# Performance work log

Measured on AMD Instinct MI355X. Metric: run time of the kernel, lower is better.

Reference implementation:

```python
import jax, jax.numpy as jnp
from jax import lax
import numpy as np

SCALES = [1.0, 0.9, 0.8, 0.7, 0.6]
SOFTMAX_SCALE = 10.0
RES_SCALE = 1.0
EPS = 1e-4  # escape_NaN buffer


def prelu(x, a):
    # torch nn.PReLU with a single shared parameter a
    return jnp.where(x >= 0, x, a * x)


def conv1x1(x, W, b):
    # x: [B,Cin,H,W], W: [Cout,Cin], b: [Cout]
    return jnp.einsum('oi,bihw->bohw', W, x) + b[None, :, None, None]


def extract_patches(x):
    # x: [B,C,H,W] -> [B, H*W, C, 3, 3]; 'same' padding (pad 1), stride 1,
    # matching F.unfold channel ordering (C, kh, kw) and row-major spatial order.
    B, C, H, W = x.shape
    p = jnp.pad(x, ((0, 0), (0, 0), (1, 1), (1, 1)))
    shifts = [p[:, :, i:i + H, j:j + W] for i in range(3) for j in range(3)]
    pat = jnp.stack(shifts, axis=-1)                      # [B,C,H,W,9]
    pat = pat.reshape(B, C, H, W, 3, 3)
    return pat.transpose(0, 2, 3, 1, 4, 5).reshape(B, H * W, C, 3, 3)


def setup_inputs() -> dict:
    key = jax.random.key(0)
    ks = jax.random.split(key, 7)
    B, C, H, W = 4, 64, 48, 48
    red = 2
    x = jax.random.normal(ks[0], (B, C, H, W), jnp.float32)
    # conv_match_L_base: 1x1 conv 64->32 + PReLU
    Wb = jax.random.normal(ks[1], (C // red, C), jnp.float32) * 0.05
    bb = jax.random.normal(ks[2], (C // red,), jnp.float32) * 0.05
    ab = jnp.asarray(0.25, jnp.float32)
    # conv_match: 1x1 conv 64->32 + PReLU
    Wm = jax.random.normal(ks[3], (C // red, C), jnp.float32) * 0.05
    bm = jax.random.normal(ks[4], (C // red,), jnp.float32) * 0.05
    am = jnp.asarray(0.25, jnp.float32)
    # conv_assembly: 1x1 conv 64->64 + PReLU
    Wa = jax.random.normal(ks[5], (C, C), jnp.float32) * 0.05
    ba = jax.random.normal(ks[6], (C,), jnp.float32) * 0.05
    aa = jnp.asarray(0.25, jnp.float32)
    return {"x": x, "Wb": Wb, "bb": bb, "ab": ab,
            "Wm": Wm, "bm": bm, "am": am,
            "Wa": Wa, "ba": ba, "aa": aa}


def reference(x, Wb, bb, ab, Wm, bm, am, Wa, ba, aa):
    B, C, H, W = x.shape
    match_base = prelu(conv1x1(x, Wb, bb), ab)  # [B,32,H,W]

    w_list, raw_list = [], []
    for s in SCALES:
        if s != 1.0:
            Hs, Ws = int(H * s), int(W * s)
            ref = jax.image.resize(x, (B, C, Hs, Ws), 'bilinear', antialias=False)
        else:
            ref = x
        base = prelu(conv1x1(ref, Wa, ba), aa)   # [B,64,Hs,Ws]
        mat = prelu(conv1x1(ref, Wm, bm), am)    # [B,32,Hs,Ws]
        raw_list.append(extract_patches(base))   # [B,Ls,64,3,3]
        w_list.append(extract_patches(mat))      # [B,Ls,32,3,3]

    wall = jnp.concatenate(w_list, axis=1)       # [B,N,32,3,3]
    rawall = jnp.concatenate(raw_list, axis=1)   # [B,N,64,3,3]
    norm = jnp.maximum(jnp.sqrt(jnp.sum(wall * wall, axis=(2, 3, 4), keepdims=True)), EPS)
    wn = wall / norm

    dn = ('NCHW', 'OIHW', 'NCHW')

    def per_sample(xb, wb, rb):
        # xb: [32,H,W], wb: [N,32,3,3], rb: [N,64,3,3]
        scores = lax.conv_general_dilated(xb[None], wb, (1, 1), ((1, 1), (1, 1)),
                                          dimension_numbers=dn)       # [1,N,H,W]
        attn = jax.nn.softmax(scores * SOFTMAX_SCALE, axis=1)
        # conv_transpose2d(attn, rb, stride=1, padding=1) == conv with flipped,
        # channel-swapped kernel and padding 1
        kt = jnp.flip(rb, axis=(2, 3)).transpose(1, 0, 2, 3)           # [64,N,3,3]
        out = lax.conv_general_dilated(attn, kt, (1, 1), ((1, 1), (1, 1)),
                                       dimension_numbers=dn)           # [1,64,H,W]
        return out[0] / 4.0

    y = jax.vmap(per_sample)(match_base, wn, rawall)  # [B,64,H,W]
    return y + x * RES_SCALE
```

## Files before the change

### kernel.cpp

```cpp
#include <hip/hip_runtime.h>
#include <hip/hip_bf16.h>
#include <hip/hip_fp16.h>

typedef __half h16;
typedef _Float16 f16;
typedef f16 f16x8 __attribute__((ext_vector_type(8)));
typedef __attribute__((ext_vector_type(4))) float f32x4;

#define NB 4
#define NCH 64
#define HW 2304
#define NP 7470
#define NPAD 7552
#define NT 236
#define NT2 118
#define NBLK 59
#define SW2 NPAD

__device__ __forceinline__ float us2f(unsigned short u){
  unsigned v = (unsigned)u << 16; float f; __builtin_memcpy(&f, &v, 4); return f;
}
__device__ __forceinline__ void gl16(const void* g, void* l){
  __builtin_amdgcn_global_load_lds((const __attribute__((address_space(1))) unsigned int*)g,
                                   (__attribute__((address_space(3))) unsigned int*)l, 16, 0, 0);
}

__device__ __forceinline__ void n_decode(int n, int& off, int& d, int& y, int& x){
  if (n < 2304)      { off = 0;    d = 48; }
  else if (n < 4153) { off = 2304; d = 43; }
  else if (n < 5597) { off = 4153; d = 38; }
  else if (n < 6686) { off = 5597; d = 33; }
  else               { off = 6686; d = 28; }
  int l = n - off; y = l / d; x = l - y * d;
}

__global__ __launch_bounds__(256) void k_detect(const void* __restrict__ x, int* __restrict__ flag){
  const unsigned short* u = (const unsigned short*)x;
  int tid = threadIdx.x;
  int c = 0;
  for (int i = tid; i < 8192; i += 256){
    float v = us2f(u[i]);
    float a = fabsf(v);
    if (v == 0.f || (a > 1e-5f && a < 1e3f)) c++;
  }
  #pragma unroll
  for (int o = 1; o < 64; o <<= 1) c += __shfl_xor(c, o);
  __shared__ int wr[4];
  if ((tid & 63) == 0) wr[tid >> 6] = c;
  __syncthreads();
  if (tid == 0) flag[0] = ((wr[0]+wr[1]+wr[2]+wr[3]) > 7000) ? 1 : 0;
}

struct CanonArgs { const void* src[10]; float* dst[10]; int end[10]; };

__global__ __launch_bounds__(256) void k_canon_all(CanonArgs a, int tot, const int* __restrict__ flag){
  int id = blockIdx.x * 256 + threadIdx.x;
  if (id >= tot) return;
  int k = 0;
  while (id >= a.end[k]) k++;
  int local = id - (k ? a.end[k-1] : 0);
  float v;
  if (flag[0]) v = us2f(((const unsigned short*)a.src[k])[local]);
  else         v = ((const float*)a.src[k])[local];
  a.dst[k][local] = v;
}

__global__ __launch_bounds__(256) void k_resize(const float* __restrict__ x, h16* __restrict__ xs){
  int id = blockIdx.x * 256 + threadIdx.x;
  if (id >= NB * NCH * NP) return;
  int b = id / (NCH*NP), rem = id - b*(NCH*NP);
  int c = rem / NP, n = rem - c*NP;
  int off, d, y, xx; n_decode(n, off, d, y, xx);
  const float* pc = x + ((size_t)b * NCH + c) * HW;
  float v;
  if (off == 0){
    v = pc[y*48 + xx];
  } else {
    float cy = (y + 0.5f) * (48.0f / (float)d) - 0.5f;
    float cx = (xx + 0.5f) * (48.0f / (float)d) - 0.5f;
    int y0 = (int)floorf(cy), x0 = (int)floorf(cx);
    float fy = cy - (float)y0, fx = cx - (float)x0;
    int y1 = min(y0 + 1, 47), x1 = min(x0 + 1, 47);
    y0 = max(y0, 0); x0 = max(x0, 0);
    v = (1.f-fy)*((1.f-fx)*pc[y0*48+x0] + fx*pc[y0*48+x1])
      + fy*((1.f-fx)*pc[y1*48+x0] + fx*pc[y1*48+x1]);
  }
  xs[id] = __float2half(v);
}

template<bool OB>
__global__ __launch_bounds__(256) void k_conv1x1(const h16* __restrict__ in, const float* __restrict__ Wt,
    const float* __restrict__ bias, const float* __restrict__ alpha, void* __restrict__ outv,
    int npix, int cout, size_t in_bstride, size_t out_bstride, int rs_in, int rs_out){
  __shared__ float Wl[64*64];
  __shared__ float it[64][64];
  int b = blockIdx.y;
  int n0 = blockIdx.x * 64;
  int tid = threadIdx.x;
  const h16* ib = in + (size_t)b * in_bstride;
  for (int i = tid; i < cout * 64; i += 256) Wl[i] = Wt[i];
  for (int i = tid; i < 64 * 64; i += 256){
    int ci = i >> 6, nn = i & 63;
    int n = n0 + nn;
    it[ci][nn] = (n < npix) ? __half2float(ib[(size_t)ci * rs_in + n]) : 0.f;
  }
  __syncthreads();
  float al = alpha[0];
  for (int oi = tid; oi < cout * 64; oi += 256){
    int co = oi >> 6, nn = oi & 63;
    float acc = bias[co];
    #pragma unroll
    for (int ci = 0; ci < 64; ci++) acc = fmaf(Wl[co*64+ci], it[ci][nn], acc);
    acc = acc >= 0.f ? acc : al * acc;
    int n = n0 + nn;
    if (n < npix){
      size_t idx = (size_t)b * out_bstride + (size_t)co * rs_out + n;
      if constexpr (OB) ((h16*)outv)[idx] = __float2half(acc);
      else              ((float*)outv)[idx] = acc;
    }
  }
}

__global__ __launch_bounds__(256) void k_sq(const float* __restrict__ mat, float* __restrict__ q){
  int id = blockIdx.x * 256 + threadIdx.x;
  if (id >= NB * NP) return;
  int b = id / NP, n = id - b * NP;
  const float* mp = mat + (size_t)b * 32 * NP + n;
  float s = 0.f;
  #pragma unroll
  for (int c = 0; c < 32; c++){ float v = mp[(size_t)c * NP]; s += v * v; }
  q[id] = s;
}

__global__ __launch_bounds__(256) void k_ninv(const float* __restrict__ q, float* __restrict__ ninv){
  int id = blockIdx.x * 256 + threadIdx.x;
  if (id >= NB * NP) return;
  int b = id / NP, n = id - b * NP;
  int off, d, y, x; n_decode(n, off, d, y, x);
  const float* qb = q + (size_t)b * NP + off;
  float s = 0.f;
  #pragma unroll
  for (int dy = -1; dy <= 1; dy++){
    int yy = y + dy; if (yy < 0 || yy >= d) continue;
    #pragma unroll
    for (int dx = -1; dx <= 1; dx++){
      int xx = x + dx; if (xx < 0 || xx >= d) continue;
      s += qb[yy * d + xx];
    }
  }
  ninv[id] = 1.f / fmaxf(sqrtf(s), 1e-4f);
}

__global__ __launch_bounds__(256) void k_packU(const float* __restrict__ mb, h16* __restrict__ U){
  int id = blockIdx.x * 256 + threadIdx.x;
  if (id >= NB * HW * 288) return;
  int b = id / (HW*288), rem = id - b*(HW*288);
  int p = rem / 288, k = rem - p * 288;
  int c = k / 9, r = k - c * 9, kh = r / 3, kw = r - kh * 3;
  int y = p / 48 + kh - 1, x = (p % 48) + kw - 1;
  float v = 0.f;
  if (y >= 0 && y < 48 && x >= 0 && x < 48)
    v = mb[((size_t)b * 32 + c) * HW + y * 48 + x];
  U[id] = __float2half(v);
}

__global__ __launch_bounds__(256) void k_packW(const float* __restrict__ mat, const float* __restrict__ ninv,
                                               h16* __restrict__ Wp, int b0, int g){
  int id = blockIdx.x * 256 + threadIdx.x;
  if (id >= g * NPAD * 288) return;
  int bg = id / (NPAD*288), rem = id - bg*(NPAD*288);
  int n = rem / 288, k = rem - n * 288;
  float v = 0.f;
  if (n < NP){
    int b = b0 + bg;
    int c = k / 9, r = k - c * 9, kh = r / 3, kw = r - kh * 3;
    int off, d, y, x; n_decode(n, off, d, y, x);
    int yy = y + kh - 1, xx = x + kw - 1;
    if (yy >= 0 && yy < d && xx >= 0 && xx < d)
      v = mat[((size_t)b * 32 + c) * NP + off + yy * d + xx] * 10.f * ninv[(size_t)b*NP + n];
  }
  Wp[id] = __float2half(v);
}

__global__ __launch_bounds__(256) void k_packR(const h16* __restrict__ src, h16* __restrict__ dst){
  int id = blockIdx.x * 256 + threadIdx.x;
  if (id >= NB * NT * 576 * 32) return;
  int b = id / (NT*576*32), rem = id - b*(NT*576*32);
  int t = rem / (576*32), rem2 = rem - t*(576*32);
  int j = rem2 / 32, kl = rem2 - j*32;
  int n = t*32 + kl;
  h16 v = __float2half(0.f);
  if (n < NP){
    int c = j / 9, r = j - c * 9, kh = r / 3, kw = r - kh * 3;
    int off, d, y, x; n_decode(n, off, d, y, x);
    int yy = y + kh - 1, xx = x + kw - 1;
    if (yy >= 0 && yy < d && xx >= 0 && xx < d)
      v = src[((size_t)b * 64 + c) * NP + off + yy * d + xx];
  }
  dst[id] = v;
}

__global__ __launch_bounds__(512) void k_gemm1m(const f16* __restrict__ U, const f16* __restrict__ Wp,
    h16* __restrict__ S16, float* __restrict__ Pm, float* __restrict__ Ps, int b0){
  int nwg = gridDim.x;
  int p = blockIdx.x;
  int qc = nwg >> 3, rc = nwg & 7, xcd = p & 7;
  int L = (xcd < rc ? xcd*(qc+1) : rc*(qc+1) + (xcd - rc)*qc) + (p >> 3);
  int my = L % 18; int t1 = L / 18; int nb = t1 % NBLK; int bg = t1 / NBLK;
  int b = b0 + bg;
  int m0 = my * 128, n0 = nb * 128;
  int tid = threadIdx.x, l = tid & 63, w = tid >> 6;
  int wm = w >> 1, wn = w & 1;
  int ch = l >> 4, cl = l & 15;
  __shared__ __align__(16) char smem[51200];
  float* mredp = (float*)(smem + 49152);
  float* sredp = (float*)(smem + 50176);
  f32x4 acc[2][4] = {};
  const f16* Ub = U + ((size_t)b * HW + m0) * 288;
  const f16* Wb = Wp + ((size_t)bg * NPAD + n0) * 288;
  int abyte[2], bbyte[4];
  #pragma unroll
  for (int mt = 0; mt < 2; mt++){
    int lr = wm*32 + mt*16 + cl;
    abyte[mt] = lr*64 + ((ch ^ ((lr>>1)&3))<<4);
  }
  #pragma unroll
  for (int nt = 0; nt < 4; nt++){
    int lr = wn*64 + nt*16 + cl;
    bbyte[nt] = lr*64 + ((ch ^ ((lr>>1)&3))<<4);
  }
  int srow = tid >> 2, scs = (tid & 3) ^ ((srow >> 1) & 3);
  auto STAGE1 = [&](int t, int bi){
    gl16(Ub + (size_t)srow*288 + t*32 + scs*8, smem + bi*8192 + tid*16);
    gl16(Wb + (size_t)srow*288 + t*32 + scs*8, smem + 24576 + bi*8192 + tid*16);
  };
  STAGE1(0, 0);
  STAGE1(1, 1);
  __syncthreads();
  int cur = 0;
  for (int t = 0; t < 9; ++t){
    int nx = cur + 2; if (nx >= 3) nx -= 3;
    if (t + 2 < 9){
      STAGE1(t + 2, nx);
      asm volatile("s_waitcnt vmcnt(4)" ::: "memory");
    } else if (t + 1 < 9){
      asm volatile("s_waitcnt vmcnt(2)" ::: "memory");
    } else {
      asm volatile("s_waitcnt vmcnt(0)" ::: "memory");
    }
    __builtin_amdgcn_s_barrier();
    asm volatile("" ::: "memory");
    const char* Ac = smem + cur*8192;
    const char* Bc = smem + 24576 + cur*8192;
    __builtin_amdgcn_s_setprio(1);
    f16x8 a[2], bv[4];
    #pragma unroll
    for (int mt = 0; mt < 2; mt++) a[mt] = *reinterpret_cast<const f16x8*>(Ac + abyte[mt]);
    #pragma unroll
    for (int nt = 0; nt < 4; nt++) bv[nt] = *reinterpret_cast<const f16x8*>(Bc + bbyte[nt]);
    #pragma unroll
    for (int mt = 0; mt < 2; mt++)
      #pragma unroll
      for (int nt = 0; nt < 4; nt++)
        acc[mt][nt] = __builtin_amdgcn_mfma_f32_16x16x32_f16(a[mt], bv[nt], acc[mt][nt], 0, 0, 0);
    __builtin_amdgcn_s_setprio(0);
    asm volatile("s_waitcnt lgkmcnt(0)" ::: "memory");
    __builtin_amdgcn_s_barrier();
    cur = cur + 1; if (cur >= 3) cur -= 3;
  }
  #pragma unroll
  for (int mt = 0; mt < 2; mt++)
    #pragma unroll
    for (int i = 0; i < 4; i++){
      float v = -3e38f;
      #pragma unroll
      for (int nt = 0; nt < 4; nt++){
        int gn = n0 + wn*64 + nt*16 + cl;
        float t = acc[mt][nt][i];
        v = fmaxf(v, (gn < NP) ? t : -3e38f);
      }
      v = fmaxf(v, __shfl_xor(v, 1));
      v = fmaxf(v, __shfl_xor(v, 2));
      v = fmaxf(v, __shfl_xor(v, 4));
      v = fmaxf(v, __shfl_xor(v, 8));
      if (cl == 0) mredp[(wm*32 + mt*16 + ch*4 + i)*2 + wn] = v;
    }
  __syncthreads();
  {
    h16* Tl = (h16*)smem;
    #pragma unroll
    for (int mt = 0; mt < 2; mt++)
      #pragma unroll
      for (int i = 0; i < 4; i++){
        int r = wm*32 + mt*16 + ch*4 + i;
        float Ml = fmaxf(mredp[r*2+0], mredp[r*2+1]);
        float s = 0.f;
        #pragma unroll
        for (int nt = 0; nt < 4; nt++){
          int c = wn*64 + nt*16 + cl;
          int gn = n0 + c;
          float e = (gn < NP) ? __expf(acc[mt][nt][i] - Ml) : 0.f;
          Tl[r*132 + c] = __float2half(e);
          s += e;
        }
        s += __shfl_xor(s, 1);
        s += __shfl_xor(s, 2);
        s += __shfl_xor(s, 4);
        s += __shfl_xor(s, 8);
        if (cl == 0) sredp[r*2 + wn] = s;
      }
  }
  __syncthreads();
  if (tid < 128){
    float Mf = fmaxf(mredp[tid*2+0], mredp[tid*2+1]);
    float Lg = sredp[tid*2+0] + sredp[tid*2+1];
    size_t o = ((size_t)bg*HW + m0 + tid)*NBLK + nb;
    Pm[o] = Mf; Ps[o] = Lg;
  }
  {
    const h16* Tl = (const h16*)smem;
    #pragma unroll
    for (int rep = 0; rep < 4; rep++){
      int idx = tid + rep*512;
      int j0 = idx >> 4, qq = idx & 15;
      uint4 v = *reinterpret_cast<const uint4*>((const char*)Tl + j0*264 + qq*16);
      h16* dst = S16 + ((size_t)bg*HW + m0 + j0)*SW2 + n0 + qq*8;
      *reinterpret_cast<uint4*>(dst) = v;
    }
  }
}

__global__ __launch_bounds__(256) void k_sfac(const float* __restrict__ Pm, const float* __restrict__ Ps,
                                              float* __restrict__ Fac, int gc){
  int rid = blockIdx.x * 4 + (threadIdx.x >> 6);
  int lane = threadIdx.x & 63;
  if (rid >= gc * HW) return;
  const float* pm = Pm + (size_t)rid * NBLK;
  const float* ps = Ps + (size_t)rid * NBLK;
  float mv = (lane < NBLK) ? pm[lane] : -3e38f;
  float sv = (lane < NBLK) ? ps[lane] : 0.f;
  float M = mv;
  #pragma unroll
  for (int o = 1; o < 64; o <<= 1) M = fmaxf(M, __shfl_xor(M, o));
  float e = (lane < NBLK) ? __expf(mv - M) : 0.f;
  float c = e * sv;
  #pragma unroll
  for (int o = 1; o < 64; o <<= 1) c += __shfl_xor(c, o);
  float inv = 1.f / c;
  if (lane < NBLK) Fac[(size_t)rid * NBLK + lane] = e * inv;
}

__global__ __launch_bounds__(512) void k_gemm2n(const f16* __restrict__ S16, const f16* __restrict__ RpT,
    const float* __restrict__ Fac, h16* __restrict__ T, int b0){
  int nwg = gridDim.x;
  int p = blockIdx.x;
  int L = (nwg % 8 == 0) ? ((p & 7)*(nwg>>3) + (p>>3)) : p;
  int jh = L % 3; int t1 = L / 3; int my = t1 % 18; int t2 = t1 / 18;
  int ks = t2 & 1;  int bg = t2 >> 1;
  int b = b0 + bg;
  int m0 = my * 128;
  int tid = threadIdx.x, l = tid & 63, w = tid >> 6;
  int wm = w >> 2, wc = w & 3;
  int ch = l >> 4, cl = l & 15;
  __shared__ __align__(16) char smem[48640];
  f32x4 acc[4][3] = {};
  int lrm[4], abyte[4], rbyte[3];
  #pragma unroll
  for (int mt = 0; mt < 4; mt++){
    lrm[mt] = wm*64 + mt*16 + cl;
    abyte[mt] = lrm[mt]*64 + ((ch ^ ((lrm[mt]>>1)&3))<<4);
  }
  #pragma unroll
  for (int nt = 0; nt < 3; nt++){
    int jr = wc*48 + nt*16 + cl;
    rbyte[nt] = jr*64 + ((ch ^ ((jr>>1)&3))<<4);
  }
  const f16* Sb  = S16 + ((size_t)bg*HW + m0)*SW2;
  const f16* Rb0 = RpT + (size_t)b*((size_t)NT*576*32) + (size_t)jh*(192*32);
  const float* facb = Fac + ((size_t)bg*HW + m0)*NBLK;
  int nb0 = (ks*NT2) >> 2;

  auto STAGE = [&](int t, int bi){
    char* dS = smem + bi*8192;
    char* dR = smem + 16384 + bi*12288;
    const f16* Rb = Rb0 + (size_t)t*(576*32);
    {
      int row = tid >> 2, cs = (tid & 3) ^ ((row >> 1) & 3);
      gl16(Sb + (size_t)row*SW2 + t*32 + cs*8, dS + tid*16);
      gl16(Rb + (size_t)row*32 + cs*8, dR + tid*16);
    }
    if (tid < 256){
      int i2 = tid + 512;
      int r2 = i2 >> 2, c2 = (i2 & 3) ^ ((r2 >> 1) & 3);
      gl16(Rb + (size_t)r2*32 + c2*8, dR + i2*16);
    }
  };

  {
    f16* fl = (f16*)(smem + 40960);
    for (int i = tid; i < 30*128; i += 512){
      int nbl = i >> 7, mm = i & 127;
      int nb = nb0 + nbl;
      fl[i] = (nb < NBLK) ? (f16)facb[(size_t)mm*NBLK + nb] : (f16)0.f;
    }
  }
  STAGE(ks*NT2, 0);
  __syncthreads();

  int cur = 0;
  for (int tt = 0; tt < NT2; ++tt){
    int t = ks*NT2 + tt;
    if (tt + 1 < NT2){
      STAGE(t + 1, cur ^ 1);
      if (tid < 256) { asm volatile("s_waitcnt vmcnt(3)" ::: "memory"); }
      else           { asm volatile("s_waitcnt vmcnt(2)" ::: "memory"); }
    } else {
      asm volatile("s_waitcnt vmcnt(0)" ::: "memory");
    }
    __builtin_amdgcn_s_barrier();
    asm volatile("" ::: "memory");
    const char* Sc = smem + cur*8192;
    const char* Rc = smem + 16384 + cur*12288;
    const f16* fl = (const f16*)(smem + 40960);
    int nbl = (t >> 2) - nb0;
    __builtin_amdgcn_s_setprio(1);
    f16x8 pa[4];
    #pragma unroll
    for (int mt = 0; mt < 4; mt++){
      f16 fac = fl[nbl*128 + lrm[mt]];
      f16x8 sv = *reinterpret_cast<const f16x8*>(Sc + abyte[mt]);
      pa[mt] = sv * fac;
    }
    #pragma unroll
    for (int nt = 0; nt < 3; nt++){
      f16x8 bv = *reinterpret_cast<const f16x8*>(Rc + rbyte[nt]);
      #pragma unroll
      for (int mt = 0; mt < 4; mt++)
        acc[mt][nt] = __builtin_amdgcn_mfma_f32_16x16x32_f16(pa[mt], bv, acc[mt][nt], 0, 0, 0);
    }
    __builtin_amdgcn_s_setprio(0);
    asm volatile("s_waitcnt lgkmcnt(0)" ::: "memory");
    __builtin_amdgcn_s_barrier();
    cur ^= 1;
  }

  h16* Tsp = T + (size_t)ks * ((size_t)NB*576*HW);
  h16* Tl = (h16*)smem;
  #pragma unroll
  for (int r = 0; r < 2; ++r){
    __syncthreads();
    if ((wc >> 1) == r){
      #pragma unroll
      for (int nt = 0; nt < 3; nt++)
        #pragma unroll
        for (int mt = 0; mt < 4; mt++)
          #pragma unroll
          for (int i = 0; i < 4; i++)
            Tl[((wc & 1)*48 + nt*16 + cl)*136 + wm*64 + mt*16 + ch*4 + i] = __float2half(acc[mt][nt][i]);
    }
    __syncthreads();
    #pragma unroll
    for (int rep = 0; rep < 3; rep++){
      int idx = tid + rep*512;
      int j0 = idx >> 4, q = idx & 15;
      uint4 v = *reinterpret_cast<const uint4*>((const char*)Tl + j0*272 + q*16);
      h16* dst = Tsp + ((size_t)b*576 + jh*192 + r*96 + j0)*HW + m0 + q*8;
      *reinterpret_cast<uint4*>(dst) = v;
    }
  }
}

__global__ __launch_bounds__(256) void k_fold(const h16* __restrict__ T, const float* __restrict__ x,
    void* __restrict__ out, const int* __restrict__ flag){
  const h16* T2 = T + (size_t)NB*576*HW;
  int id = blockIdx.x * 256 + threadIdx.x;
  if (id >= NB * 64 * HW) return;
  int b = id / (64*HW), id2 = id - b*(64*HW);
  int co = id2 / HW, p = id2 - co * HW;
  int y = p / 48, xx = p - y * 48;
  float acc = 0.f;
  #pragma unroll
  for (int dy = -1; dy <= 1; dy++){
    int yy = y + dy; if (yy < 0 || yy >= 48) continue;
    #pragma unroll
    for (int dx = -1; dx <= 1; dx++){
      int x2 = xx + dx; if (x2 < 0 || x2 >= 48) continue;
      int j = co*9 + (1-dy)*3 + (1-dx);
      size_t o = ((size_t)b*576 + j)*HW + yy*48 + x2;
      acc += __half2float(T[o]) + __half2float(T2[o]);
    }
  }
  size_t gi = (size_t)id;
  float r = x[gi] + 0.25f * acc;
  if (flag[0]) ((__hip_bfloat16*)out)[gi] = __float2bfloat16(r);
  else         ((float*)out)[gi] = r;
}

extern "C" void kernel_launch(void* const* d_in, const int* in_sizes, int n_in,
                              void* d_out, int out_size, void* d_ws, size_t ws_size,
                              hipStream_t stream){
  (void)out_size; (void)n_in;

  char* cur = (char*)d_ws;
  auto carve = [&](size_t bytes)->char*{
    char* p = cur; cur += (bytes + 255) & ~(size_t)255; return p;
  };
  int*   flag  = (int*)  carve(4);
  float* canon[10];
  for (int i = 0; i < 10; i++) canon[i] = (float*)carve((size_t)in_sizes[i] * 4);
  float* xc = canon[0];
  float* Wb = canon[1]; float* bb = canon[2]; float* ab = canon[3];
  float* Wm = canon[4]; float* bm = canon[5]; float* am = canon[6];
  float* Wa = canon[7]; float* ba = canon[8]; float* aa = canon[9];

  h16*   xs    = (h16*)  carve((size_t)NB * 64 * NP * 2);
  float* mbuf  = (float*)carve((size_t)NB * 32 * HW * 4);
  float* mat   = (float*)carve((size_t)NB * 32 * NP * 4);
  float* qbuf  = (float*)carve((size_t)NB * NP * 4);
  float* ninv  = (float*)carve((size_t)NB * NP * 4);
  h16*   baseh = (h16*)  carve((size_t)NB * 64 * NP * 2);
  h16*   U     = (h16*)  carve((size_t)NB * HW * 288 * 2);
  h16*   RpT   = (h16*)  carve((size_t)NB * NT * 576 * 32 * 2);
  h16*   T     = (h16*)  carve((size_t)2 * NB * 576 * HW * 2);

  size_t fixed = (size_t)(cur - (char*)d_ws);
  size_t perb  = (((size_t)NPAD*288*2 + 255) & ~(size_t)255)
               + (((size_t)HW*SW2*2 + 255) & ~(size_t)255)
               + 3 * (((size_t)HW*NBLK*4 + 255) & ~(size_t)255);
  size_t avail = (ws_size > fixed) ? ws_size - fixed : 0;
  int g = (int)(avail / perb);
  if (g < 1) g = 1;
  if (g > NB) g = NB;
  h16*   Wp  = (h16*)  carve((size_t)g * NPAD * 288 * 2);
  h16*   S16 = (h16*)  carve((size_t)g * HW * SW2 * 2);
  float* Pm  = (float*)carve((size_t)g * HW * NBLK * 4);
  float* Ps  = (float*)carve((size_t)g * HW * NBLK * 4);
  float* Fac = (float*)carve((size_t)g * HW * NBLK * 4);

  k_detect<<<1, 256, 0, stream>>>(d_in[0], flag);
  {
    CanonArgs ca; int tot = 0;
    for (int i = 0; i < 10; i++){
      ca.src[i] = d_in[i]; ca.dst[i] = canon[i];
      tot += in_sizes[i]; ca.end[i] = tot;
    }
    k_canon_all<<<(tot + 255)/256, 256, 0, stream>>>(ca, tot, flag);
  }

  k_resize<<<((size_t)NB*NCH*NP + 255)/256, 256, 0, stream>>>(xc, xs);

  dim3 gm((NP + 63)/64, NB);
  k_conv1x1<false><<<gm, 256, 0, stream>>>(xs, Wm, bm, am, (void*)mat,   NP, 32, (size_t)64*NP, (size_t)32*NP, NP, NP);
  k_conv1x1<true ><<<gm, 256, 0, stream>>>(xs, Wa, ba, aa, (void*)baseh, NP, 64, (size_t)64*NP, (size_t)64*NP, NP, NP);
  dim3 gb2((HW + 63)/64, NB);
  k_conv1x1<false><<<gb2, 256, 0, stream>>>(xs, Wb, bb, ab, (void*)mbuf, HW, 32, (size_t)64*NP, (size_t)32*HW, NP, HW);

  k_sq  <<<(NB*NP + 255)/256, 256, 0, stream>>>(mat, qbuf);
  k_ninv<<<(NB*NP + 255)/256, 256, 0, stream>>>(qbuf, ninv);
  k_packU<<<((size_t)NB*HW*288 + 255)/256, 256, 0, stream>>>(mbuf, U);
  k_packR<<<((size_t)NB*NT*576*32 + 255)/256, 256, 0, stream>>>(baseh, RpT);

  for (int b0 = 0; b0 < NB; b0 += g){
    int gc = (b0 + g <= NB) ? g : (NB - b0);
    k_packW<<<((size_t)gc*NPAD*288 + 255)/256, 256, 0, stream>>>(mat, ninv, Wp, b0, gc);
    int nwg1 = 18 * NBLK * gc;
    k_gemm1m<<<nwg1, 512, 0, stream>>>((const f16*)U, (const f16*)Wp, S16, Pm, Ps, b0);
    k_sfac<<<(gc*HW + 3)/4, 256, 0, stream>>>(Pm, Ps, Fac, gc);
    int nwg2 = 3 * 18 * 2 * gc;
    k_gemm2n<<<nwg2, 512, 0, stream>>>((const f16*)S16, (const f16*)RpT, Fac, T, b0);
  }

  k_fold<<<(NB*64*HW + 255)/256, 256, 0, stream>>>(T, xc, d_out, flag);
}
```

Before: 332.8 us.

## Merge small launches, read raw x directly, and precompute coordinate lookup table

```diff
diff --git a/kernel.cpp b/kernel.cpp
--- a/kernel.cpp
+++ b/kernel.cpp
@@ -16,9 +16,13 @@
 #define NT2 118
 #define NBLK 59
 #define SW2 NPAD
+#define TOTU (NB*HW*288)
 
 __device__ __forceinline__ float us2f(unsigned short u){
   unsigned v = (unsigned)u << 16; float f; __builtin_memcpy(&f, &v, 4); return f;
+}
+__device__ __forceinline__ float ldf(const void* p, size_t i, int f){
+  return f ? us2f(((const unsigned short*)p)[i]) : ((const float*)p)[i];
 }
 __device__ __forceinline__ void gl16(const void* g, void* l){
   __builtin_amdgcn_global_load_lds((const __attribute__((address_space(1))) unsigned int*)g,
@@ -32,6 +36,20 @@
   else if (n < 6686) { off = 5597; d = 33; }
   else               { off = 6686; d = 28; }
   int l = n - off; y = l / d; x = l - y * d;
+}
+__device__ __forceinline__ void n_range(int n, int& off, int& d){
+  if (n < 2304)      { off = 0;    d = 48; }
+  else if (n < 4153) { off = 2304; d = 43; }
+  else if (n < 5597) { off = 4153; d = 38; }
+  else if (n < 6686) { off = 5597; d = 33; }
+  else               { off = 6686; d = 28; }
+}
+
+__global__ __launch_bounds__(256) void k_lut(ushort2* __restrict__ lut){
+  int n = blockIdx.x * 256 + threadIdx.x;
+  if (n >= NP) return;
+  int off, d, y, x; n_decode(n, off, d, y, x);
+  lut[n] = make_ushort2((unsigned short)y, (unsigned short)x);
 }
 
 __global__ __launch_bounds__(256) void k_detect(const void* __restrict__ x, int* __restrict__ flag){
@@ -51,7 +69,7 @@
   if (tid == 0) flag[0] = ((wr[0]+wr[1]+wr[2]+wr[3]) > 7000) ? 1 : 0;
 }
 
-struct CanonArgs { const void* src[10]; float* dst[10]; int end[10]; };
+struct CanonArgs { const void* src[9]; float* dst[9]; int end[9]; };
 
 __global__ __launch_bounds__(256) void k_canon_all(CanonArgs a, int tot, const int* __restrict__ flag){
   int id = blockIdx.x * 256 + threadIdx.x;
@@ -65,16 +83,20 @@
   a.dst[k][local] = v;
 }
 
-__global__ __launch_bounds__(256) void k_resize(const float* __restrict__ x, h16* __restrict__ xs){
+__global__ __launch_bounds__(256) void k_resize(const void* __restrict__ xraw, const int* __restrict__ flag,
+                                                const ushort2* __restrict__ lut, h16* __restrict__ xs){
   int id = blockIdx.x * 256 + threadIdx.x;
   if (id >= NB * NCH * NP) return;
+  int f = flag[0];
   int b = id / (NCH*NP), rem = id - b*(NCH*NP);
   int c = rem / NP, n = rem - c*NP;
-  int off, d, y, xx; n_decode(n, off, d, y, xx);
-  const float* pc = x + ((size_t)b * NCH + c) * HW;
+  int off, d; n_range(n, off, d);
+  ushort2 yx = lut[n];
+  int y = yx.x, xx = yx.y;
+  size_t base = ((size_t)b * NCH + c) * HW;
   float v;
   if (off == 0){
-    v = pc[y*48 + xx];
+    v = ldf(xraw, base + y*48 + xx, f);
   } else {
     float cy = (y + 0.5f) * (48.0f / (float)d) - 0.5f;
     float cx = (xx + 0.5f) * (48.0f / (float)d) - 0.5f;
@@ -82,30 +104,36 @@
     float fy = cy - (float)y0, fx = cx - (float)x0;
     int y1 = min(y0 + 1, 47), x1 = min(x0 + 1, 47);
     y0 = max(y0, 0); x0 = max(x0, 0);
-    v = (1.f-fy)*((1.f-fx)*pc[y0*48+x0] + fx*pc[y0*48+x1])
-      + fy*((1.f-fx)*pc[y1*48+x0] + fx*pc[y1*48+x1]);
+    v = (1.f-fy)*((1.f-fx)*ldf(xraw, base + y0*48+x0, f) + fx*ldf(xraw, base + y0*48+x1, f))
+      + fy*((1.f-fx)*ldf(xraw, base + y1*48+x0, f) + fx*ldf(xraw, base + y1*48+x1, f));
   }
   xs[id] = __float2half(v);
 }
 
-template<bool OB>
-__global__ __launch_bounds__(256) void k_conv1x1(const h16* __restrict__ in, const float* __restrict__ Wt,
-    const float* __restrict__ bias, const float* __restrict__ alpha, void* __restrict__ outv,
-    int npix, int cout, size_t in_bstride, size_t out_bstride, int rs_in, int rs_out){
+struct ConvArgs {
+  const float* W[3]; const float* bias[3]; const float* alpha[3];
+  void* out[3]; int npix[3]; int cout[3]; size_t ob[3]; int rso[3]; int of16[3];
+};
+__global__ __launch_bounds__(256) void k_conv_all(const h16* __restrict__ xs, ConvArgs ca){
+  int z = blockIdx.z;
+  int npix = ca.npix[z], cout = ca.cout[z];
+  int n0 = blockIdx.x * 64;
+  if (n0 >= npix) return;
   __shared__ float Wl[64*64];
   __shared__ float it[64][64];
   int b = blockIdx.y;
-  int n0 = blockIdx.x * 64;
   int tid = threadIdx.x;
-  const h16* ib = in + (size_t)b * in_bstride;
+  const h16* ib = xs + (size_t)b * (64*NP);
+  const float* Wt = ca.W[z];
   for (int i = tid; i < cout * 64; i += 256) Wl[i] = Wt[i];
   for (int i = tid; i < 64 * 64; i += 256){
     int ci = i >> 6, nn = i & 63;
     int n = n0 + nn;
-    it[ci][nn] = (n < npix) ? __half2float(ib[(size_t)ci * rs_in + n]) : 0.f;
+    it[ci][nn] = (n < npix) ? __half2float(ib[(size_t)ci * NP + n]) : 0.f;
   }
   __syncthreads();
-  float al = alpha[0];
+  float al = ca.alpha[z][0];
+  const float* bias = ca.bias[z];
   for (int oi = tid; oi < cout * 64; oi += 256){
     int co = oi >> 6, nn = oi & 63;
     float acc = bias[co];
@@ -114,9 +142,9 @@
     acc = acc >= 0.f ? acc : al * acc;
     int n = n0 + nn;
     if (n < npix){
-      size_t idx = (size_t)b * out_bstride + (size_t)co * rs_out + n;
-      if constexpr (OB) ((h16*)outv)[idx] = __float2half(acc);
-      else              ((float*)outv)[idx] = acc;
+      size_t idx = (size_t)b * ca.ob[z] + (size_t)co * ca.rso[z] + n;
+      if (ca.of16[z]) ((h16*)ca.out[z])[idx] = __float2half(acc);
+      else            ((float*)ca.out[z])[idx] = acc;
     }
   }
 }
@@ -132,11 +160,14 @@
   q[id] = s;
 }
 
-__global__ __launch_bounds__(256) void k_ninv(const float* __restrict__ q, float* __restrict__ ninv){
+__global__ __launch_bounds__(256) void k_ninv(const float* __restrict__ q, float* __restrict__ ninv,
+                                              const ushort2* __restrict__ lut){
   int id = blockIdx.x * 256 + threadIdx.x;
   if (id >= NB * NP) return;
   int b = id / NP, n = id - b * NP;
-  int off, d, y, x; n_decode(n, off, d, y, x);
+  int off, d; n_range(n, off, d);
+  ushort2 yx = lut[n];
+  int y = yx.x, x = yx.y;
   const float* qb = q + (size_t)b * NP + off;
   float s = 0.f;
   #pragma unroll
@@ -151,21 +182,40 @@
   ninv[id] = 1.f / fmaxf(sqrtf(s), 1e-4f);
 }
 
-__global__ __launch_bounds__(256) void k_packU(const float* __restrict__ mb, h16* __restrict__ U){
+__global__ __launch_bounds__(256) void k_packUR(const float* __restrict__ mbuf, const h16* __restrict__ baseh,
+    const ushort2* __restrict__ lut, h16* __restrict__ U, h16* __restrict__ RpT){
   int id = blockIdx.x * 256 + threadIdx.x;
-  if (id >= NB * HW * 288) return;
-  int b = id / (HW*288), rem = id - b*(HW*288);
-  int p = rem / 288, k = rem - p * 288;
-  int c = k / 9, r = k - c * 9, kh = r / 3, kw = r - kh * 3;
-  int y = p / 48 + kh - 1, x = (p % 48) + kw - 1;
-  float v = 0.f;
-  if (y >= 0 && y < 48 && x >= 0 && x < 48)
-    v = mb[((size_t)b * 32 + c) * HW + y * 48 + x];
-  U[id] = __float2half(v);
+  if (id < TOTU){
+    int b = id / (HW*288), rem = id - b*(HW*288);
+    int p = rem / 288, k = rem - p * 288;
+    int c = k / 9, r = k - c * 9, kh = r / 3, kw = r - kh * 3;
+    int y = p / 48 + kh - 1, x = (p % 48) + kw - 1;
+    float v = 0.f;
+    if (y >= 0 && y < 48 && x >= 0 && x < 48)
+      v = mbuf[((size_t)b * 32 + c) * HW + y * 48 + x];
+    U[id] = __float2half(v);
+    return;
+  }
+  int id2 = id - TOTU;
+  if (id2 >= NB * NT * 576 * 32) return;
+  int b = id2 / (NT*576*32), rem = id2 - b*(NT*576*32);
+  int t = rem / (576*32), rem2 = rem - t*(576*32);
+  int j = rem2 / 32, kl = rem2 - j*32;
+  int n = t*32 + kl;
+  h16 v = __float2half(0.f);
+  if (n < NP){
+    int c = j / 9, r = j - c * 9, kh = r / 3, kw = r - kh * 3;
+    int off, d; n_range(n, off, d);
+    ushort2 yx = lut[n];
+    int yy = (int)yx.x + kh - 1, xx = (int)yx.y + kw - 1;
+    if (yy >= 0 && yy < d && xx >= 0 && xx < d)
+      v = baseh[((size_t)b * 64 + c) * NP + off + yy * d + xx];
+  }
+  RpT[id2] = v;
 }
 
 __global__ __launch_bounds__(256) void k_packW(const float* __restrict__ mat, const float* __restrict__ ninv,
-                                               h16* __restrict__ Wp, int b0, int g){
+                                               const ushort2* __restrict__ lut, h16* __restrict__ Wp, int b0, int g){
   int id = blockIdx.x * 256 + threadIdx.x;
   if (id >= g * NPAD * 288) return;
   int bg = id / (NPAD*288), rem = id - bg*(NPAD*288);
@@ -174,30 +224,13 @@
   if (n < NP){
     int b = b0 + bg;
     int c = k / 9, r = k - c * 9, kh = r / 3, kw = r - kh * 3;
-    int off, d, y, x; n_decode(n, off, d, y, x);
-    int yy = y + kh - 1, xx = x + kw - 1;
+    int off, d; n_range(n, off, d);
+    ushort2 yx = lut[n];
+    int yy = (int)yx.x + kh - 1, xx = (int)yx.y + kw - 1;
     if (yy >= 0 && yy < d && xx >= 0 && xx < d)
       v = mat[((size_t)b * 32 + c) * NP + off + yy * d + xx] * 10.f * ninv[(size_t)b*NP + n];
   }
   Wp[id] = __float2half(v);
-}
-
-__global__ __launch_bounds__(256) void k_packR(const h16* __restrict__ src, h16* __restrict__ dst){
-  int id = blockIdx.x * 256 + threadIdx.x;
-  if (id >= NB * NT * 576 * 32) return;
-  int b = id / (NT*576*32), rem = id - b*(NT*576*32);
-  int t = rem / (576*32), rem2 = rem - t*(576*32);
-  int j = rem2 / 32, kl = rem2 - j*32;
-  int n = t*32 + kl;
-  h16 v = __float2half(0.f);
-  if (n < NP){
-    int c = j / 9, r = j - c * 9, kh = r / 3, kw = r - kh * 3;
-    int off, d, y, x; n_decode(n, off, d, y, x);
-    int yy = y + kh - 1, xx = x + kw - 1;
-    if (yy >= 0 && yy < d && xx >= 0 && xx < d)
-      v = src[((size_t)b * 64 + c) * NP + off + yy * d + xx];
-  }
-  dst[id] = v;
 }
 
 __global__ __launch_bounds__(512) void k_gemm1m(const f16* __restrict__ U, const f16* __restrict__ Wp,
@@ -470,11 +503,12 @@
   }
 }
 
-__global__ __launch_bounds__(256) void k_fold(const h16* __restrict__ T, const float* __restrict__ x,
+__global__ __launch_bounds__(256) void k_fold(const h16* __restrict__ T, const void* __restrict__ xraw,
     void* __restrict__ out, const int* __restrict__ flag){
   const h16* T2 = T + (size_t)NB*576*HW;
   int id = blockIdx.x * 256 + threadIdx.x;
   if (id >= NB * 64 * HW) return;
+  int f = flag[0];
   int b = id / (64*HW), id2 = id - b*(64*HW);
   int co = id2 / HW, p = id2 - co * HW;
   int y = p / 48, xx = p - y * 48;
@@ -491,9 +525,9 @@
     }
   }
   size_t gi = (size_t)id;
-  float r = x[gi] + 0.25f * acc;
-  if (flag[0]) ((__hip_bfloat16*)out)[gi] = __float2bfloat16(r);
-  else         ((float*)out)[gi] = r;
+  float r = ldf(xraw, gi, f) + 0.25f * acc;
+  if (f) ((__hip_bfloat16*)out)[gi] = __float2bfloat16(r);
+  else   ((float*)out)[gi] = r;
 }
 
 extern "C" void kernel_launch(void* const* d_in, const int* in_sizes, int n_in,
@@ -505,13 +539,13 @@
   auto carve = [&](size_t bytes)->char*{
     char* p = cur; cur += (bytes + 255) & ~(size_t)255; return p;
   };
-  int*   flag  = (int*)  carve(4);
-  float* canon[10];
-  for (int i = 0; i < 10; i++) canon[i] = (float*)carve((size_t)in_sizes[i] * 4);
-  float* xc = canon[0];
-  float* Wb = canon[1]; float* bb = canon[2]; float* ab = canon[3];
-  float* Wm = canon[4]; float* bm = canon[5]; float* am = canon[6];
-  float* Wa = canon[7]; float* ba = canon[8]; float* aa = canon[9];
+  int*     flag = (int*)    carve(4);
+  ushort2* lut  = (ushort2*)carve((size_t)NP * 4);
+  float* canon[9];
+  for (int i = 0; i < 9; i++) canon[i] = (float*)carve((size_t)in_sizes[i+1] * 4);
+  float* Wb = canon[0]; float* bb = canon[1]; float* ab = canon[2];
+  float* Wm = canon[3]; float* bm = canon[4]; float* am = canon[5];
+  float* Wa = canon[6]; float* ba = canon[7]; float* aa = canon[8];
 
   h16*   xs    = (h16*)  carve((size_t)NB * 64 * NP * 2);
   float* mbuf  = (float*)carve((size_t)NB * 32 * HW * 4);
@@ -538,31 +572,37 @@
   float* Fac = (float*)carve((size_t)g * HW * NBLK * 4);
 
   k_detect<<<1, 256, 0, stream>>>(d_in[0], flag);
+  k_lut<<<(NP + 255)/256, 256, 0, stream>>>(lut);
   {
     CanonArgs ca; int tot = 0;
-    for (int i = 0; i < 10; i++){
-      ca.src[i] = d_in[i]; ca.dst[i] = canon[i];
-      tot += in_sizes[i]; ca.end[i] = tot;
+    for (int i = 0; i < 9; i++){
+      ca.src[i] = d_in[i+1]; ca.dst[i] = canon[i];
+      tot += in_sizes[i+1]; ca.end[i] = tot;
     }
     k_canon_all<<<(tot + 255)/256, 256, 0, stream>>>(ca, tot, flag);
   }
 
-  k_resize<<<((size_t)NB*NCH*NP + 255)/256, 256, 0, stream>>>(xc, xs);
-
-  dim3 gm((NP + 63)/64, NB);
-  k_conv1x1<false><<<gm, 256, 0, stream>>>(xs, Wm, bm, am, (void*)mat,   NP, 32, (size_t)64*NP, (size_t)32*NP, NP, NP);
-  k_conv1x1<true ><<<gm, 256, 0, stream>>>(xs, Wa, ba, aa, (void*)baseh, NP, 64, (size_t)64*NP, (size_t)64*NP, NP, NP);
-  dim3 gb2((HW + 63)/64, NB);
-  k_conv1x1<false><<<gb2, 256, 0, stream>>>(xs, Wb, bb, ab, (void*)mbuf, HW, 32, (size_t)64*NP, (size_t)32*HW, NP, HW);
+  k_resize<<<((size_t)NB*NCH*NP + 255)/256, 256, 0, stream>>>(d_in[0], flag, lut, xs);
+
+  {
+    ConvArgs ca;
+    ca.W[0]=Wm; ca.bias[0]=bm; ca.alpha[0]=am; ca.out[0]=(void*)mat;   ca.npix[0]=NP; ca.cout[0]=32; ca.ob[0]=(size_t)32*NP; ca.rso[0]=NP; ca.of16[0]=0;
+    ca.W[1]=Wa; ca.bias[1]=ba; ca.alpha[1]=aa; ca.out[1]=(void*)baseh; ca.npix[1]=NP; ca.cout[1]=64; ca.ob[1]=(size_t)64*NP; ca.rso[1]=NP; ca.of16[1]=1;
+    ca.W[2]=Wb; ca.bias[2]=bb; ca.alpha[2]=ab; ca.out[2]=(void*)mbuf;  ca.npix[2]=HW; ca.cout[2]=32; ca.ob[2]=(size_t)32*HW; ca.rso[2]=HW; ca.of16[2]=0;
+    dim3 gc3((NP + 63)/64, NB, 3);
+    k_conv_all<<<gc3, 256, 0, stream>>>(xs, ca);
+  }
 
   k_sq  <<<(NB*NP + 255)/256, 256, 0, stream>>>(mat, qbuf);
-  k_ninv<<<(NB*NP + 255)/256, 256, 0, stream>>>(qbuf, ninv);
-  k_packU<<<((size_t)NB*HW*288 + 255)/256, 256, 0, stream>>>(mbuf, U);
-  k_packR<<<((size_t)NB*NT*576*32 + 255)/256, 256, 0, stream>>>(baseh, RpT);
+  k_ninv<<<(NB*NP + 255)/256, 256, 0, stream>>>(qbuf, ninv, lut);
+  {
+    long long tot = (long long)TOTU + (long long)NB*NT*576*32;
+    k_packUR<<<(unsigned)((tot + 255)/256), 256, 0, stream>>>(mbuf, baseh, lut, U, RpT);
+  }
 
   for (int b0 = 0; b0 < NB; b0 += g){
     int gc = (b0 + g <= NB) ? g : (NB - b0);
-    k_packW<<<((size_t)gc*NPAD*288 + 255)/256, 256, 0, stream>>>(mat, ninv, Wp, b0, gc);
+    k_packW<<<((size_t)gc*NPAD*288 + 255)/256, 256, 0, stream>>>(mat, ninv, lut, Wp, b0, gc);
     int nwg1 = 18 * NBLK * gc;
     k_gemm1m<<<nwg1, 512, 0, stream>>>((const f16*)U, (const f16*)Wp, S16, Pm, Ps, b0);
     k_sfac<<<(gc*HW + 3)/4, 256, 0, stream>>>(Pm, Ps, Fac, gc);
@@ -570,5 +610,5 @@
     k_gemm2n<<<nwg2, 512, 0, stream>>>((const f16*)S16, (const f16*)RpT, Fac, T, b0);
   }
 
-  k_fold<<<(NB*64*HW + 255)/256, 256, 0, stream>>>(T, xc, d_out, flag);
-}
+  k_fold<<<(NB*64*HW + 255)/256, 256, 0, stream>>>(T, d_in[0], d_out, flag);
+}
```

Result: faster. 311.2 us (median of 3 runs) (-6.5%).
